# Optimization experiments

Measured on AMD Instinct MI355X. Metric: run time of the kernel, lower is better.

Reference implementation:

```python
import jax, jax.numpy as jnp
import numpy as np

DIM = 1024
HEADS = 16
DIM_HEAD = DIM // HEADS  # 64
B, N = 4, 1024


def setup_inputs() -> dict:
    key = jax.random.key(0)
    ks = jax.random.split(key, 8)
    s = 1.0 / np.sqrt(DIM)
    inp = {
        "x": jax.random.normal(ks[0], (B, N, DIM), dtype=jnp.float32),
        # weights stored as [in, out] so y = x @ W (+ b), equivalent to torch Linear
        "Wq": jax.random.normal(ks[1], (DIM, DIM), dtype=jnp.float32) * s,
        "Wk": jax.random.normal(ks[2], (DIM, DIM), dtype=jnp.float32) * s,
        "Wv": jax.random.normal(ks[3], (DIM, DIM), dtype=jnp.float32) * s,
        "Wproj": jax.random.normal(ks[4], (DIM, DIM), dtype=jnp.float32) * s,
        "bproj": jnp.zeros((DIM,), dtype=jnp.float32),
        "Wpre": jax.random.normal(ks[5], (DIM, DIM), dtype=jnp.float32) * s,
        "bpre": jnp.zeros((DIM,), dtype=jnp.float32),
        # original init is -inf (non-runnable); use a finite trained value
        "pi": jnp.full((1,), 0.5, dtype=jnp.float32),
    }
    return inp


def reference(x, Wq, Wk, Wv, Wproj, bproj, Wpre, bpre, pi):
    b, n, c = x.shape
    h, dh = HEADS, DIM_HEAD
    residual = x
    # bias-logit path: Linear -> SiLU -> bmm with itself (dropout p=0 is identity)
    pre = jax.nn.silu(x @ Wpre + bpre)                       # [B,N,C]
    logits = jnp.einsum('bnc,bmc->bnm', pre, pre) / jnp.sqrt(jnp.float32(c))
    # QKV (x2 defaults to x)
    q = (x @ Wq).reshape(b, n, h, dh).transpose(0, 2, 1, 3)  # [B,H,N,Dh]
    k = (x @ Wk).reshape(b, n, h, dh).transpose(0, 2, 1, 3)
    v = (x @ Wv).reshape(b, n, h, dh).transpose(0, 2, 1, 3)
    score = jnp.einsum('bhnd,bhmd->bhnm', q, k) / jnp.sqrt(jnp.float32(dh))
    final_logits = pi[0] * logits[:, None, :, :] + score     # broadcast bias over heads
    attn = jax.nn.softmax(final_logits, axis=-1)
    out = jnp.einsum('bhnm,bhmd->bhnd', attn, v)             # [B,H,N,Dh]
    out = out.transpose(0, 2, 1, 3).reshape(b, n, h * dh)
    out = out @ Wproj + bproj
    return out + residual
```

## Files before the change

kernel.cpp:

```cpp
#include <hip/hip_runtime.h>

using bf16x8 = __attribute__((ext_vector_type(8))) short;
using v8bf   = __attribute__((ext_vector_type(8))) __bf16;
using f32x4  = __attribute__((ext_vector_type(4))) float;
using u32x2  = __attribute__((ext_vector_type(2))) unsigned;
using bf16x2 = __attribute__((ext_vector_type(2))) __bf16;

typedef const __attribute__((address_space(1))) void GASV;
typedef __attribute__((address_space(3))) void LASV;

template <typename V>
__device__ __forceinline__ auto mfma_bf16_impl(V a, V b, f32x4 c, int)
    -> decltype(__builtin_amdgcn_mfma_f32_16x16x32_bf16(a, b, c, 0, 0, 0)) {
  return __builtin_amdgcn_mfma_f32_16x16x32_bf16(a, b, c, 0, 0, 0);
}
template <typename V>
__device__ __forceinline__ f32x4 mfma_bf16_impl(V a, V b, f32x4 c, long) {
  return __builtin_amdgcn_mfma_f32_16x16x32_bf16(
      __builtin_bit_cast(v8bf, a), __builtin_bit_cast(v8bf, b), c, 0, 0, 0);
}
__device__ __forceinline__ f32x4 MFMA(bf16x8 a, bf16x8 b, f32x4 c) {
  return mfma_bf16_impl(a, b, c, 0);
}

__device__ __forceinline__ void async_lds16(const void* g, void* l) {
  __builtin_amdgcn_global_load_lds((GASV*)g, (LASV*)l, 16, 0, 0);
}

__device__ __forceinline__ unsigned short f2bf(float x) {
  unsigned u = __float_as_uint(x);
  u = u + 0x7fffu + ((u >> 16) & 1u);
  return (unsigned short)(u >> 16);
}

__device__ __forceinline__ unsigned pack_bf2(float lo, float hi) {
  bf16x2 t;
  t[0] = (__bf16)lo;
  t[1] = (__bf16)hi;
  return __builtin_bit_cast(unsigned, t);
}

#define LOG2E 1.4426950408889634f
#define SOFT_OFF 14.0f

__global__ __launch_bounds__(256) void k_prep(
    const float4* __restrict__ x, ushort4* __restrict__ xb,
    const float* __restrict__ w0, const float* __restrict__ w1,
    const float* __restrict__ w2, const float* __restrict__ w3,
    const float* __restrict__ w4, unsigned short* __restrict__ out) {
  const int bid = blockIdx.x, tid = threadIdx.x;
  if (bid < 4096) {
    const int i = bid * 256 + tid;
    float4 v = x[i];
    ushort4 p;
    p.x = f2bf(v.x); p.y = f2bf(v.y); p.z = f2bf(v.z); p.w = f2bf(v.w);
    xb[i] = p;
    return;
  }
  __shared__ float t[32][33];
  const int tb = bid - 4096;
  const int z = tb >> 10;
  const float* W = (z == 0) ? w0 : (z == 1) ? w1 : (z == 2) ? w2 : (z == 3) ? w3 : w4;
  const float sc = (z == 1) ? (LOG2E / 8.0f) : 1.0f;
  unsigned short* o = out + (size_t)z * (1u << 20);
  const int bx = (tb & 31) * 32, by = ((tb >> 5) & 31) * 32;
  const int tx = tid & 31, ty = tid >> 5;
#pragma unroll
  for (int i = 0; i < 4; ++i)
    t[ty + i * 8][tx] = W[(size_t)(by + ty + i * 8) * 1024 + bx + tx];
  __syncthreads();
#pragma unroll
  for (int i = 0; i < 4; ++i)
    o[(size_t)(bx + ty + i * 8) * 1024 + by + tx] = f2bf(t[tx][ty + i * 8] * sc);
}

template <int MI, int NI>
__device__ __forceinline__ void gemm_core_t(const unsigned short* __restrict__ A,
                                            const unsigned short* __restrict__ Bt,
                                            unsigned short* ldsA,
                                            unsigned short* ldsB,
                                            f32x4 acc[MI][NI]) {
  const int tid = threadIdx.x;
  const int w = tid >> 6, lane = tid & 63;
  const int lane15 = lane & 15, quad = lane >> 4;
  const int wm = w >> 1, wn = w & 1;
  for (int ko = 0; ko < 16; ++ko) {
    __syncthreads();
#pragma unroll
    for (int i = 0; i < MI; ++i) {
      const int p = i * 256 + tid;
      const int r = p >> 3, cc = (p & 7) ^ (r & 7);
      async_lds16(A + r * 1024 + ko * 64 + cc * 8, ldsA + (i * 256 + w * 64) * 8);
    }
#pragma unroll
    for (int i = 0; i < NI; ++i) {
      const int p = i * 256 + tid;
      const int r = p >> 3, cc = (p & 7) ^ (r & 7);
      async_lds16(Bt + r * 1024 + ko * 64 + cc * 8, ldsB + (i * 256 + w * 64) * 8);
    }
    __syncthreads();
    bf16x8 af[MI][2], bfr[NI][2];
#pragma unroll
    for (int t = 0; t < MI; ++t) {
      const int row = wm * (MI * 16) + t * 16 + lane15;
#pragma unroll
      for (int h = 0; h < 2; ++h)
        af[t][h] = *(const bf16x8*)&ldsA[row * 64 + (((h * 4 + quad) ^ (row & 7)) << 3)];
    }
#pragma unroll
    for (int t = 0; t < NI; ++t) {
      const int row = wn * (NI * 16) + t * 16 + lane15;
#pragma unroll
      for (int h = 0; h < 2; ++h)
        bfr[t][h] = *(const bf16x8*)&ldsB[row * 64 + (((h * 4 + quad) ^ (row & 7)) << 3)];
    }
#pragma unroll
    for (int mi = 0; mi < MI; ++mi)
#pragma unroll
      for (int ni = 0; ni < NI; ++ni) {
        acc[mi][ni] = MFMA(af[mi][0], bfr[ni][0], acc[mi][ni]);
        acc[mi][ni] = MFMA(af[mi][1], bfr[ni][1], acc[mi][ni]);
      }
  }
}

#define GEMM_PROLOGUE(MI_, NI_)                                      \
  __shared__ unsigned short ldsA[(MI_)*32 * 64];                     \
  __shared__ unsigned short ldsB[(NI_)*32 * 64];                     \
  f32x4 acc[MI_][NI_];                                               \
  {                                                                  \
    f32x4 z_ = {0.f, 0.f, 0.f, 0.f};                                 \
    for (int i_ = 0; i_ < (MI_); ++i_)                               \
      for (int j_ = 0; j_ < (NI_); ++j_) acc[i_][j_] = z_;           \
  }

#define GEMM_EPI_IDX(MI_, NI_)                                       \
  const int tid = threadIdx.x, w = tid >> 6, lane = tid & 63;        \
  const int lane15 = lane & 15, quad = lane >> 4;                    \
  const int wm = w >> 1, wn = w & 1;                                 \
  const int r0 = tm + wm * ((MI_)*16) + quad * 4;                    \
  const int c0 = tn + wn * ((NI_)*16) + lane15;

__global__ __launch_bounds__(512, 4) void k_gemm_qkvpre(
    const unsigned short* __restrict__ xb, const unsigned short* __restrict__ wt,
    const float* __restrict__ bpre, unsigned short* __restrict__ pre,
    unsigned short* __restrict__ qb, unsigned short* __restrict__ kb,
    unsigned short* __restrict__ vt) {
  __shared__ unsigned short ldsA[2][256 * 32];
  __shared__ unsigned short ldsB[2][128 * 32];
  const int bid = blockIdx.x;
  const int xcd = bid & 7, idx = bid >> 3;
  const int z = xcd >> 1, half = xcd & 1;
  int tm, tn;
  if (z == 3) {
    tm = half * 2048 + (idx >> 3) * 256;
    tn = (idx & 7) * 128;
  } else {
    tm = (idx >> 4) * 256;
    tn = half * 2048 + (idx & 15) * 128;
  }
  const unsigned short* At =
      (z == 3) ? xb + (size_t)tm * 1024
               : wt + (size_t)z * (1u << 20) + (size_t)tm * 1024;
  const unsigned short* Bt_ =
      (z == 3) ? wt + (size_t)3 * (1u << 20) + (size_t)tn * 1024
               : xb + (size_t)tn * 1024;

  const int tid = threadIdx.x, w = tid >> 6, lane = tid & 63;
  const int lane15 = lane & 15, quad = lane >> 4;
  const int wm = w >> 1, wn = w & 1;

  f32x4 acc[4][4];
  {
    f32x4 z_ = {0.f, 0.f, 0.f, 0.f};
#pragma unroll
    for (int i = 0; i < 4; ++i)
#pragma unroll
      for (int j = 0; j < 4; ++j) acc[i][j] = z_;
  }

  auto stage = [&](int ko, int buf) {
#pragma unroll
    for (int j = 0; j < 2; ++j) {
      const int p = j * 512 + tid;
      const int r = p >> 2, cc = (p & 3) ^ ((r >> 1) & 3);
      async_lds16(At + (size_t)r * 1024 + ko * 32 + cc * 8,
                  &ldsA[buf][(j * 512 + w * 64) * 8]);
    }
    {
      const int p = tid;
      const int r = p >> 2, cc = (p & 3) ^ ((r >> 1) & 3);
      async_lds16(Bt_ + (size_t)r * 1024 + ko * 32 + cc * 8,
                  &ldsB[buf][(w * 64) * 8]);
    }
  };

  stage(0, 0);
  __syncthreads();
  for (int t = 0; t < 32; ++t) {
    const int buf = t & 1;
    if (t + 1 < 32) stage(t + 1, buf ^ 1);
    const unsigned short* sA = ldsA[buf];
    const unsigned short* sB = ldsB[buf];
    bf16x8 af[4], bf[4];
#pragma unroll
    for (int mi = 0; mi < 4; ++mi) {
      const int row = wm * 64 + mi * 16 + lane15;
      af[mi] = *(const bf16x8*)&sA[row * 32 + ((quad ^ ((row >> 1) & 3)) << 3)];
    }
#pragma unroll
    for (int ni = 0; ni < 4; ++ni) {
      const int row = wn * 64 + ni * 16 + lane15;
      bf[ni] = *(const bf16x8*)&sB[row * 32 + ((quad ^ ((row >> 1) & 3)) << 3)];
    }
    __builtin_amdgcn_s_setprio(1);
#pragma unroll
    for (int mi = 0; mi < 4; ++mi)
#pragma unroll
      for (int ni = 0; ni < 4; ++ni)
        acc[mi][ni] = MFMA(af[mi], bf[ni], acc[mi][ni]);
    __builtin_amdgcn_s_setprio(0);
    __syncthreads();
  }

  const int r0 = tm + wm * 64 + quad * 4;
  const int c0 = tn + wn * 64 + lane15;
  if (z == 0) {
#pragma unroll
    for (int mf = 0; mf < 4; ++mf) {
      const float4 b4 = *(const float4*)&bpre[r0 + mf * 16];
#pragma unroll
      for (int nf = 0; nf < 4; ++nf) {
        const int seq = c0 + nf * 16;
        float vv[4];
#pragma unroll
        for (int rr = 0; rr < 4; ++rr) {
          float v = acc[mf][nf][rr] + ((const float*)&b4)[rr];
          vv[rr] = v / (1.0f + __expf(-v));
        }
        ushort4 pk;
        pk.x = f2bf(vv[0]); pk.y = f2bf(vv[1]);
        pk.z = f2bf(vv[2]); pk.w = f2bf(vv[3]);
        *(ushort4*)&pre[(size_t)seq * 1024 + r0 + mf * 16] = pk;
      }
    }
  } else if (z == 1 || z == 2) {
    unsigned short* dst = (z == 1) ? qb : kb;
#pragma unroll
    for (int mf = 0; mf < 4; ++mf)
#pragma unroll
      for (int nf = 0; nf < 4; ++nf) {
        const int seq = c0 + nf * 16;
        ushort4 pk;
        pk.x = f2bf(acc[mf][nf][0]); pk.y = f2bf(acc[mf][nf][1]);
        pk.z = f2bf(acc[mf][nf][2]); pk.w = f2bf(acc[mf][nf][3]);
        *(ushort4*)&dst[(size_t)seq * 1024 + r0 + mf * 16] = pk;
      }
  } else {
#pragma unroll
    for (int mf = 0; mf < 4; ++mf) {
      const int m = r0 + mf * 16;
      const int bb_ = m >> 10, nseq = m & 1023;
#pragma unroll
      for (int nf = 0; nf < 4; ++nf) {
        const int cg = c0 + nf * 16;
        const int hh = cg >> 6, dd = cg & 63;
        ushort4 pk;
        pk.x = f2bf(acc[mf][nf][0]); pk.y = f2bf(acc[mf][nf][1]);
        pk.z = f2bf(acc[mf][nf][2]); pk.w = f2bf(acc[mf][nf][3]);
        *(ushort4*)&vt[(size_t)(((bb_ * 16 + hh) << 6) + dd) * 1024 + nseq] = pk;
      }
    }
  }
}

__global__ __launch_bounds__(256) void k_gemm_logits(
    const unsigned short* __restrict__ pre, const float* __restrict__ pi,
    unsigned short* __restrict__ lg) {
  const int bz = blockIdx.z;
  const unsigned short* base = pre + ((size_t)bz << 20);
  const int tm = blockIdx.y * 64, tn = blockIdx.x * 128;
  GEMM_PROLOGUE(2, 4);
  gemm_core_t<2, 4>(base + (size_t)tm * 1024, base + (size_t)tn * 1024, ldsA, ldsB, acc);
  const float sc = pi[0] * (LOG2E / 32.0f);
  GEMM_EPI_IDX(2, 4);
#pragma unroll
  for (int mi = 0; mi < 2; ++mi)
#pragma unroll
    for (int ni = 0; ni < 4; ++ni) {
      const int col = c0 + ni * 16;
      ushort4 pk;
      pk.x = f2bf(acc[mi][ni][0] * sc); pk.y = f2bf(acc[mi][ni][1] * sc);
      pk.z = f2bf(acc[mi][ni][2] * sc); pk.w = f2bf(acc[mi][ni][3] * sc);
      *(ushort4*)&lg[((size_t)bz << 20) + (size_t)col * 1024 + r0 + mi * 16] = pk;
    }
}

__global__ __launch_bounds__(256) void k_gemm_out(
    const unsigned short* __restrict__ ao, const unsigned short* __restrict__ wtp,
    const float* __restrict__ bproj, const float* __restrict__ xres,
    float* __restrict__ out) {
  const int tm = blockIdx.x * 64, tn = blockIdx.y * 128;
  GEMM_PROLOGUE(2, 4);
  gemm_core_t<2, 4>(wtp + (size_t)tm * 1024, ao + (size_t)tn * 1024, ldsA, ldsB, acc);
  GEMM_EPI_IDX(2, 4);
#pragma unroll
  for (int mi = 0; mi < 2; ++mi) {
    const float4 b4 = *(const float4*)&bproj[r0 + mi * 16];
#pragma unroll
    for (int ni = 0; ni < 4; ++ni) {
      const int seq = c0 + ni * 16;
      const size_t idx = (size_t)seq * 1024 + r0 + mi * 16;
      const float4 rv = *(const float4*)&xres[idx];
      float4 ov;
      ov.x = acc[mi][ni][0] + b4.x + rv.x;
      ov.y = acc[mi][ni][1] + b4.y + rv.y;
      ov.z = acc[mi][ni][2] + b4.z + rv.z;
      ov.w = acc[mi][ni][3] + b4.w + rv.w;
      *(float4*)&out[idx] = ov;
    }
  }
}

__global__ __launch_bounds__(256, 4) void k_attn(
    const unsigned short* __restrict__ qb, const unsigned short* __restrict__ kb,
    const unsigned short* __restrict__ vt, const unsigned short* __restrict__ lg,
    unsigned short* __restrict__ ao) {
  __shared__ unsigned short ldsK[2 * 64 * 64];
  __shared__ unsigned short ldsV[2 * 64 * 64];
  const int bid = blockIdx.x;
  const int xcd = bid & 7, idx = bid >> 3;
  const int b = xcd >> 1, hg = xcd & 1;
  const int h = hg * 8 + (idx >> 4);
  const int q0 = (idx & 15) * 64;
  const int tid = threadIdx.x, w = tid >> 6, lane = tid & 63;
  const int lane15 = lane & 15, quad = lane >> 4;
  const int qw = q0 + w * 16;

  bf16x8 qf[2];
  {
    const unsigned short* qrow =
        qb + (size_t)((b << 10) + qw + lane15) * 1024 + (h << 6);
    qf[0] = *(const bf16x8*)(qrow + quad * 8);
    qf[1] = *(const bf16x8*)(qrow + 32 + quad * 8);
  }
  const unsigned short* kbase = kb + ((size_t)(b << 10)) * 1024 + (h << 6);
  const unsigned short* vbase = vt + ((size_t)((b * 16 + h) << 6)) * 1024;
  const unsigned short* lgrow =
      lg + ((size_t)b << 20) + (size_t)(qw + lane15) * 1024 +
      (quad >> 1) * 16 + (quad & 1) * 4;

  float lcol = 0.f;
  f32x4 o[4];
  {
    f32x4 z_ = {0.f, 0.f, 0.f, 0.f};
#pragma unroll
    for (int nt = 0; nt < 4; ++nt) o[nt] = z_;
  }

  uint2 lgc[4], lgn[4];

  auto stage = [&](int ch, unsigned short* sK, unsigned short* sV) {
    const int kv0 = ch * 64;
#pragma unroll
    for (int i = 0; i < 2; ++i) {
      const int p = i * 256 + tid;
      const int r = p >> 3, cc = (p & 7) ^ (r & 7);
      const int rk = (r & 0x27) | ((r & 8) << 1) | ((r & 16) >> 1);
      async_lds16(kbase + (size_t)(kv0 + rk) * 1024 + cc * 8,
                  sK + (i * 256 + w * 64) * 8);
      async_lds16(vbase + (size_t)r * 1024 + kv0 + cc * 8,
                  sV + (i * 256 + w * 64) * 8);
    }
  };
  auto lgload = [&](int ch, uint2 dst[4]) {
#pragma unroll
    for (int mi = 0; mi < 4; ++mi)
      dst[mi] = *(const uint2*)(lgrow + ch * 64 + (mi >> 1) * 32 + (mi & 1) * 8);
  };
  auto compute = [&](const unsigned short* sK, const unsigned short* sV) {
    f32x4 s[4];
    __builtin_amdgcn_s_setprio(1);
#pragma unroll
    for (int mi = 0; mi < 4; ++mi) {
      const int row = mi * 16 + lane15;
      bf16x8 k0 = *(const bf16x8*)&sK[row * 64 + ((quad ^ (row & 7)) << 3)];
      bf16x8 k1 = *(const bf16x8*)&sK[row * 64 + (((4 + quad) ^ (row & 7)) << 3)];
      f32x4 t;
      t[0] = __uint_as_float(lgc[mi].x << 16);
      t[1] = __uint_as_float(lgc[mi].x & 0xffff0000u);
      t[2] = __uint_as_float(lgc[mi].y << 16);
      t[3] = __uint_as_float(lgc[mi].y & 0xffff0000u);
      t = MFMA(k0, qf[0], t);
      t = MFMA(k1, qf[1], t);
      s[mi] = t;
    }
    __builtin_amdgcn_s_setprio(0);
    float rs = 0.f;
    uint2 pk[4];
#pragma unroll
    for (int mi = 0; mi < 4; ++mi) {
      const float p0 = __builtin_amdgcn_exp2f(s[mi][0] - SOFT_OFF);
      const float p1 = __builtin_amdgcn_exp2f(s[mi][1] - SOFT_OFF);
      const float p2 = __builtin_amdgcn_exp2f(s[mi][2] - SOFT_OFF);
      const float p3 = __builtin_amdgcn_exp2f(s[mi][3] - SOFT_OFF);
      rs += (p0 + p1) + (p2 + p3);
      pk[mi].x = pack_bf2(p0, p1);
      pk[mi].y = pack_bf2(p2, p3);
    }
    lcol += rs;

#pragma unroll
    for (int kp = 0; kp < 2; ++kp) {
      u32x2 rx = __builtin_amdgcn_permlane16_swap(pk[2 * kp].x, pk[2 * kp + 1].x, 0, 0);
      u32x2 ry = __builtin_amdgcn_permlane16_swap(pk[2 * kp].y, pk[2 * kp + 1].y, 0, 0);
      uint4 bfv;
      bfv.x = rx.x;
      bfv.y = ry.x;
      bfv.z = rx.y;
      bfv.w = ry.y;
      const bf16x8 pf = __builtin_bit_cast(bf16x8, bfv);
      __builtin_amdgcn_s_setprio(1);
#pragma unroll
      for (int dt = 0; dt < 4; ++dt) {
        const int d = dt * 16 + lane15;
        bf16x8 vf = *(const bf16x8*)&sV[d * 64 +
                                        (((kp * 4 + quad) ^ (d & 7)) << 3)];
        o[dt] = MFMA(vf, pf, o[dt]);
      }
      __builtin_amdgcn_s_setprio(0);
    }
  };

  unsigned short* sK0 = ldsK;
  unsigned short* sK1 = ldsK + 64 * 64;
  unsigned short* sV0 = ldsV;
  unsigned short* sV1 = ldsV + 64 * 64;

  stage(0, sK0, sV0);
  lgload(0, lgc);
  __syncthreads();

  for (int c = 0; c < 16; c += 2) {
    stage(c + 1, sK1, sV1);
    lgload(c + 1, lgn);
    compute(sK0, sV0);
    __syncthreads();
#pragma unroll
    for (int mi = 0; mi < 4; ++mi) lgc[mi] = lgn[mi];
    if (c + 2 < 16) {
      stage(c + 2, sK0, sV0);
      lgload(c + 2, lgn);
    }
    compute(sK1, sV1);
    __syncthreads();
#pragma unroll
    for (int mi = 0; mi < 4; ++mi) lgc[mi] = lgn[mi];
  }

  lcol += __shfl_xor(lcol, 16);
  lcol += __shfl_xor(lcol, 32);
  const float rinv = 1.0f / lcol;
  const int m = (b << 10) + qw + lane15;
#pragma unroll
  for (int dt = 0; dt < 4; ++dt) {
    ushort4 pkk;
    pkk.x = f2bf(o[dt][0] * rinv);
    pkk.y = f2bf(o[dt][1] * rinv);
    pkk.z = f2bf(o[dt][2] * rinv);
    pkk.w = f2bf(o[dt][3] * rinv);
    *(ushort4*)&ao[(size_t)m * 1024 + (h << 6) + dt * 16 + quad * 4] = pkk;
  }
}

extern "C" void kernel_launch(void* const* d_in, const int* in_sizes, int n_in,
                              void* d_out, int out_size, void* d_ws, size_t ws_size,
                              hipStream_t stream) {
  const float* x     = (const float*)d_in[0];
  const float* Wq    = (const float*)d_in[1];
  const float* Wk    = (const float*)d_in[2];
  const float* Wv    = (const float*)d_in[3];
  const float* Wproj = (const float*)d_in[4];
  const float* bproj = (const float*)d_in[5];
  const float* Wpre  = (const float*)d_in[6];
  const float* bpre  = (const float*)d_in[7];
  const float* pi    = (const float*)d_in[8];
  float* out = (float*)d_out;
  char* ws = (char*)d_ws;

  unsigned short* xb  = (unsigned short*)(ws);
  unsigned short* wt  = (unsigned short*)(ws + (8u << 20));
  unsigned short* pre = (unsigned short*)(ws + (18u << 20));
  unsigned short* qb  = (unsigned short*)(ws + (26u << 20));
  unsigned short* kb  = (unsigned short*)(ws + (34u << 20));
  unsigned short* vt  = (unsigned short*)(ws + (42u << 20));
  unsigned short* lg  = xb;
  unsigned short* ao  = pre;

  k_prep<<<dim3(4096 + 5120), dim3(256), 0, stream>>>(
      (const float4*)x, (ushort4*)xb, Wpre, Wq, Wk, Wv, Wproj, wt);
  k_gemm_qkvpre<<<dim3(512), dim3(512), 0, stream>>>(xb, wt, bpre, pre, qb, kb, vt);
  k_gemm_logits<<<dim3(8, 16, 4), dim3(256), 0, stream>>>(pre, pi, lg);
  k_attn<<<dim3(1024), dim3(256), 0, stream>>>(qb, kb, vt, lg, ao);
  k_gemm_out<<<dim3(16, 32, 1), dim3(256), 0, stream>>>(ao, wt + 4 * (1u << 20), bproj, x, out);
}
```

Baseline: 210.9 us.

## Process two query sub-tiles per wave in attention to reuse K/V fragments

Each wave of the attention kernel now handles 32 query rows instead of 16, so every K and V fragment read from LDS feeds two sets of MFMAs. The grid is halved to 512 blocks of 128 queries, and launch bounds drop to 2 blocks per SM to allow more registers. This cuts LDS reads and K/V staging traffic per query row. In exchange it raises register pressure, lowers occupancy, and leaves fewer blocks to fill the device.

```diff
diff --git a/kernel.cpp b/kernel.cpp
--- a/kernel.cpp
+++ b/kernel.cpp
@@ -322,7 +322,7 @@
   }
 }
 
-__global__ __launch_bounds__(256, 4) void k_attn(
+__global__ __launch_bounds__(256, 2) void k_attn(
     const unsigned short* __restrict__ qb, const unsigned short* __restrict__ kb,
     const unsigned short* __restrict__ vt, const unsigned short* __restrict__ lg,
     unsigned short* __restrict__ ao) {
@@ -331,18 +331,19 @@
   const int bid = blockIdx.x;
   const int xcd = bid & 7, idx = bid >> 3;
   const int b = xcd >> 1, hg = xcd & 1;
-  const int h = hg * 8 + (idx >> 4);
-  const int q0 = (idx & 15) * 64;
+  const int h = hg * 8 + (idx >> 3);
+  const int q0 = (idx & 7) * 128;
   const int tid = threadIdx.x, w = tid >> 6, lane = tid & 63;
   const int lane15 = lane & 15, quad = lane >> 4;
-  const int qw = q0 + w * 16;
-
-  bf16x8 qf[2];
-  {
+  const int qw = q0 + w * 32;
+
+  bf16x8 qf[2][2];
+#pragma unroll
+  for (int qh = 0; qh < 2; ++qh) {
     const unsigned short* qrow =
-        qb + (size_t)((b << 10) + qw + lane15) * 1024 + (h << 6);
-    qf[0] = *(const bf16x8*)(qrow + quad * 8);
-    qf[1] = *(const bf16x8*)(qrow + 32 + quad * 8);
+        qb + (size_t)((b << 10) + qw + qh * 16 + lane15) * 1024 + (h << 6);
+    qf[qh][0] = *(const bf16x8*)(qrow + quad * 8);
+    qf[qh][1] = *(const bf16x8*)(qrow + 32 + quad * 8);
   }
   const unsigned short* kbase = kb + ((size_t)(b << 10)) * 1024 + (h << 6);
   const unsigned short* vbase = vt + ((size_t)((b * 16 + h) << 6)) * 1024;
@@ -350,15 +351,17 @@
       lg + ((size_t)b << 20) + (size_t)(qw + lane15) * 1024 +
       (quad >> 1) * 16 + (quad & 1) * 4;
 
-  float lcol = 0.f;
-  f32x4 o[4];
+  float lcol[2] = {0.f, 0.f};
+  f32x4 o[2][4];
   {
     f32x4 z_ = {0.f, 0.f, 0.f, 0.f};
 #pragma unroll
-    for (int nt = 0; nt < 4; ++nt) o[nt] = z_;
-  }
-
-  uint2 lgc[4], lgn[4];
+    for (int qh = 0; qh < 2; ++qh)
+#pragma unroll
+      for (int nt = 0; nt < 4; ++nt) o[qh][nt] = z_;
+  }
+
+  uint2 lgc[2][4], lgn[2][4];
 
   auto stage = [&](int ch, unsigned short* sK, unsigned short* sV) {
     const int kv0 = ch * 64;
@@ -373,62 +376,79 @@
                   sV + (i * 256 + w * 64) * 8);
     }
   };
-  auto lgload = [&](int ch, uint2 dst[4]) {
-#pragma unroll
-    for (int mi = 0; mi < 4; ++mi)
-      dst[mi] = *(const uint2*)(lgrow + ch * 64 + (mi >> 1) * 32 + (mi & 1) * 8);
+  auto lgload = [&](int ch, uint2 dst[2][4]) {
+#pragma unroll
+    for (int qh = 0; qh < 2; ++qh)
+#pragma unroll
+      for (int mi = 0; mi < 4; ++mi)
+        dst[qh][mi] = *(const uint2*)(lgrow + qh * 16 * 1024 + ch * 64 +
+                                      (mi >> 1) * 32 + (mi & 1) * 8);
   };
   auto compute = [&](const unsigned short* sK, const unsigned short* sV) {
-    f32x4 s[4];
+    f32x4 s[2][4];
     __builtin_amdgcn_s_setprio(1);
 #pragma unroll
     for (int mi = 0; mi < 4; ++mi) {
       const int row = mi * 16 + lane15;
       bf16x8 k0 = *(const bf16x8*)&sK[row * 64 + ((quad ^ (row & 7)) << 3)];
       bf16x8 k1 = *(const bf16x8*)&sK[row * 64 + (((4 + quad) ^ (row & 7)) << 3)];
-      f32x4 t;
-      t[0] = __uint_as_float(lgc[mi].x << 16);
-      t[1] = __uint_as_float(lgc[mi].x & 0xffff0000u);
-      t[2] = __uint_as_float(lgc[mi].y << 16);
-      t[3] = __uint_as_float(lgc[mi].y & 0xffff0000u);
-      t = MFMA(k0, qf[0], t);
-      t = MFMA(k1, qf[1], t);
-      s[mi] = t;
+#pragma unroll
+      for (int qh = 0; qh < 2; ++qh) {
+        f32x4 t;
+        t[0] = __uint_as_float(lgc[qh][mi].x << 16);
+        t[1] = __uint_as_float(lgc[qh][mi].x & 0xffff0000u);
+        t[2] = __uint_as_float(lgc[qh][mi].y << 16);
+        t[3] = __uint_as_float(lgc[qh][mi].y & 0xffff0000u);
+        t = MFMA(k0, qf[qh][0], t);
+        t = MFMA(k1, qf[qh][1], t);
+        s[qh][mi] = t;
+      }
     }
     __builtin_amdgcn_s_setprio(0);
-    float rs = 0.f;
-    uint2 pk[4];
-#pragma unroll
-    for (int mi = 0; mi < 4; ++mi) {
-      const float p0 = __builtin_amdgcn_exp2f(s[mi][0] - SOFT_OFF);
-      const float p1 = __builtin_amdgcn_exp2f(s[mi][1] - SOFT_OFF);
-      const float p2 = __builtin_amdgcn_exp2f(s[mi][2] - SOFT_OFF);
-      const float p3 = __builtin_amdgcn_exp2f(s[mi][3] - SOFT_OFF);
-      rs += (p0 + p1) + (p2 + p3);
-      pk[mi].x = pack_bf2(p0, p1);
-      pk[mi].y = pack_bf2(p2, p3);
-    }
-    lcol += rs;
+    uint2 pk[2][4];
+#pragma unroll
+    for (int qh = 0; qh < 2; ++qh) {
+      float rs = 0.f;
+#pragma unroll
+      for (int mi = 0; mi < 4; ++mi) {
+        const float p0 = __builtin_amdgcn_exp2f(s[qh][mi][0] - SOFT_OFF);
+        const float p1 = __builtin_amdgcn_exp2f(s[qh][mi][1] - SOFT_OFF);
+        const float p2 = __builtin_amdgcn_exp2f(s[qh][mi][2] - SOFT_OFF);
+        const float p3 = __builtin_amdgcn_exp2f(s[qh][mi][3] - SOFT_OFF);
+        rs += (p0 + p1) + (p2 + p3);
+        pk[qh][mi].x = pack_bf2(p0, p1);
+        pk[qh][mi].y = pack_bf2(p2, p3);
+      }
+      lcol[qh] += rs;
+    }
 
 #pragma unroll
     for (int kp = 0; kp < 2; ++kp) {
-      u32x2 rx = __builtin_amdgcn_permlane16_swap(pk[2 * kp].x, pk[2 * kp + 1].x, 0, 0);
-      u32x2 ry = __builtin_amdgcn_permlane16_swap(pk[2 * kp].y, pk[2 * kp + 1].y, 0, 0);
-      uint4 bfv;
-      bfv.x = rx.x;
-      bfv.y = ry.x;
-      bfv.z = rx.y;
-      bfv.w = ry.y;
-      const bf16x8 pf = __builtin_bit_cast(bf16x8, bfv);
-      __builtin_amdgcn_s_setprio(1);
+      bf16x8 vf[4];
 #pragma unroll
       for (int dt = 0; dt < 4; ++dt) {
         const int d = dt * 16 + lane15;
-        bf16x8 vf = *(const bf16x8*)&sV[d * 64 +
-                                        (((kp * 4 + quad) ^ (d & 7)) << 3)];
-        o[dt] = MFMA(vf, pf, o[dt]);
-      }
-      __builtin_amdgcn_s_setprio(0);
+        vf[dt] = *(const bf16x8*)&sV[d * 64 +
+                                     (((kp * 4 + quad) ^ (d & 7)) << 3)];
+      }
+#pragma unroll
+      for (int qh = 0; qh < 2; ++qh) {
+        u32x2 rx = __builtin_amdgcn_permlane16_swap(pk[qh][2 * kp].x,
+                                                    pk[qh][2 * kp + 1].x, 0, 0);
+        u32x2 ry = __builtin_amdgcn_permlane16_swap(pk[qh][2 * kp].y,
+                                                    pk[qh][2 * kp + 1].y, 0, 0);
+        uint4 bfv;
+        bfv.x = rx.x;
+        bfv.y = ry.x;
+        bfv.z = rx.y;
+        bfv.w = ry.y;
+        const bf16x8 pf = __builtin_bit_cast(bf16x8, bfv);
+        __builtin_amdgcn_s_setprio(1);
+#pragma unroll
+        for (int dt = 0; dt < 4; ++dt)
+          o[qh][dt] = MFMA(vf[dt], pf, o[qh][dt]);
+        __builtin_amdgcn_s_setprio(0);
+      }
     }
   };
 
@@ -447,7 +467,9 @@
     compute(sK0, sV0);
     __syncthreads();
 #pragma unroll
-    for (int mi = 0; mi < 4; ++mi) lgc[mi] = lgn[mi];
+    for (int qh = 0; qh < 2; ++qh)
+#pragma unroll
+      for (int mi = 0; mi < 4; ++mi) lgc[qh][mi] = lgn[qh][mi];
     if (c + 2 < 16) {
       stage(c + 2, sK0, sV0);
       lgload(c + 2, lgn);
@@ -455,21 +477,27 @@
     compute(sK1, sV1);
     __syncthreads();
 #pragma unroll
-    for (int mi = 0; mi < 4; ++mi) lgc[mi] = lgn[mi];
-  }
-
-  lcol += __shfl_xor(lcol, 16);
-  lcol += __shfl_xor(lcol, 32);
-  const float rinv = 1.0f / lcol;
-  const int m = (b << 10) + qw + lane15;
-#pragma unroll
-  for (int dt = 0; dt < 4; ++dt) {
-    ushort4 pkk;
-    pkk.x = f2bf(o[dt][0] * rinv);
-    pkk.y = f2bf(o[dt][1] * rinv);
-    pkk.z = f2bf(o[dt][2] * rinv);
-    pkk.w = f2bf(o[dt][3] * rinv);
-    *(ushort4*)&ao[(size_t)m * 1024 + (h << 6) + dt * 16 + quad * 4] = pkk;
+    for (int qh = 0; qh < 2; ++qh)
+#pragma unroll
+      for (int mi = 0; mi < 4; ++mi) lgc[qh][mi] = lgn[qh][mi];
+  }
+
+#pragma unroll
+  for (int qh = 0; qh < 2; ++qh) {
+    float lc = lcol[qh];
+    lc += __shfl_xor(lc, 16);
+    lc += __shfl_xor(lc, 32);
+    const float rinv = 1.0f / lc;
+    const int m = (b << 10) + qw + qh * 16 + lane15;
+#pragma unroll
+    for (int dt = 0; dt < 4; ++dt) {
+      ushort4 pkk;
+      pkk.x = f2bf(o[qh][dt][0] * rinv);
+      pkk.y = f2bf(o[qh][dt][1] * rinv);
+      pkk.z = f2bf(o[qh][dt][2] * rinv);
+      pkk.w = f2bf(o[qh][dt][3] * rinv);
+      *(ushort4*)&ao[(size_t)m * 1024 + (h << 6) + dt * 16 + quad * 4] = pkk;
+    }
   }
 }
 
@@ -501,6 +529,6 @@
       (const float4*)x, (ushort4*)xb, Wpre, Wq, Wk, Wv, Wproj, wt);
   k_gemm_qkvpre<<<dim3(512), dim3(512), 0, stream>>>(xb, wt, bpre, pre, qb, kb, vt);
   k_gemm_logits<<<dim3(8, 16, 4), dim3(256), 0, stream>>>(pre, pi, lg);
-  k_attn<<<dim3(1024), dim3(256), 0, stream>>>(qb, kb, vt, lg, ao);
+  k_attn<<<dim3(512), dim3(256), 0, stream>>>(qb, kb, vt, lg, ao);
   k_gemm_out<<<dim3(16, 32, 1), dim3(256), 0, stream>>>(ao, wt + 4 * (1u << 20), bproj, x, out);
 }
```

Measured after the change: 209.2 us. No clear change (-0.8%).
